# Kernel optimization log

Hardware: AMD Instinct MI355X
Metric: run time of the kernel (lower is better)

## Reference

```python
import jax, jax.numpy as jnp
import numpy as np

N_NODES = 50000
N_EDGES = 800000
NEG_SLOPE = 0.2  # PyG GATv2Conv default
EPS = 1e-16      # PyG softmax denominator epsilon


def _segment_softmax(logits, seg, num_segments):
    # logits: [E, H]; seg: [E] target-node ids
    m = jax.ops.segment_max(logits, seg, num_segments=num_segments)
    p = jnp.exp(logits - m[seg])
    s = jax.ops.segment_sum(p, seg, num_segments=num_segments)
    return p / (s[seg] + EPS)


def _gatv2_conv(x, src, dst, Wl, Wr, att, bias, heads, out_ch, concat):
    # x: [N, F]; Wl/Wr: [F, heads*out_ch]; att: [heads, out_ch]
    n = x.shape[0]
    xl = (x @ Wl).reshape(n, heads, out_ch)
    xr = (x @ Wr).reshape(n, heads, out_ch)
    # GATv2: e_ij = att . leaky_relu(xl[j] + xr[i]) for edge j->i
    e = jax.nn.leaky_relu(xl[src] + xr[dst], NEG_SLOPE)  # [E, H, C]
    logit = jnp.einsum('ehc,hc->eh', e, att)             # [E, H]
    alpha = _segment_softmax(logit, dst, n)              # [E, H]
    out = jax.ops.segment_sum(alpha[:, :, None] * xl[src], dst, num_segments=n)  # [N, H, C]
    if concat:
        out = out.reshape(n, heads * out_ch)
    else:
        out = out.mean(axis=1)
    return out + bias


def setup_inputs() -> dict:
    key = jax.random.key(0)
    ks = jax.random.split(key, 20)
    in_ch, hid, out_ch, heads, edge_dim = 128, 128, 64, 8, 6
    c1 = hid // heads  # 16
    g = lambda k, shp, fan: (jax.random.normal(k, shp, jnp.float32) / np.sqrt(fan)).astype(jnp.float32)
    inp = {
        'x': jax.random.normal(ks[0], (N_NODES, in_ch), jnp.float32),
        'edge_index': jax.random.randint(ks[1], (2, N_EDGES), 0, N_NODES, dtype=jnp.int64),
        'edge_attr': jax.random.normal(ks[2], (N_EDGES, edge_dim), jnp.float32),
        'Wl1': g(ks[3], (in_ch, heads * c1), in_ch),
        'Wr1': g(ks[4], (in_ch, heads * c1), in_ch),
        'att1': g(ks[5], (heads, c1), c1),
        'b1': jnp.zeros((heads * c1,), jnp.float32),
        # layer 2: GATv2Conv(hid -> out_ch, heads=1, no concat)
        'Wl2': g(ks[6], (hid, out_ch), hid),
        'Wr2': g(ks[7], (hid, out_ch), hid),
        'att2': g(ks[8], (1, out_ch), out_ch),
        'b2': jnp.zeros((out_ch,), jnp.float32),
        # edge encoder (computed but unused downstream, as in the source)
        'We1': g(ks[9], (edge_dim, hid), edge_dim), 'be1': jnp.zeros((hid,), jnp.float32),
        'We2': g(ks[10], (hid, hid), hid), 'be2': jnp.zeros((hid,), jnp.float32),
        # classifier
        'Wc1': g(ks[11], (out_ch, hid), out_ch), 'bc1': jnp.zeros((hid,), jnp.float32),
        'Wc2': g(ks[12], (hid, 2), hid), 'bc2': jnp.zeros((2,), jnp.float32),
    }
    return inp


def reference(x, edge_index, edge_attr, Wl1, Wr1, att1, b1, Wl2, Wr2, att2, b2,
              We1, be1, We2, be2, Wc1, bc1, Wc2, bc2):
    n = x.shape[0]
    # edge encoder (dead code in the original forward; kept for fidelity)
    _edge_feats = jax.nn.relu(edge_attr @ We1 + be1) @ We2 + be2
    # add self-loops (PyG GATv2Conv default add_self_loops=True)
    loop = jnp.arange(n, dtype=edge_index.dtype)
    src = jnp.concatenate([edge_index[0], loop])
    dst = jnp.concatenate([edge_index[1], loop])
    # layer 1 (heads=8, concat) + relu; dropout is identity in eval
    h = _gatv2_conv(x, src, dst, Wl1, Wr1, att1, b1, heads=8, out_ch=16, concat=True)
    h = jax.nn.relu(h)
    # layer 2 (heads=1, mean)
    emb = _gatv2_conv(h, src, dst, Wl2, Wr2, att2, b2, heads=1, out_ch=64, concat=False)
    logits = jax.nn.relu(emb @ Wc1 + bc1) @ Wc2 + bc2
    return emb, logits
```

## Files before the change

kernel.cpp:

```cpp
#include <hip/hip_runtime.h>
#include <hip/hip_bf16.h>
#include <cfloat>

#define N_NODES 50000
#define N_EDGES 800000
#define E_TOT   850000
#define NEG_SLOPE 0.2f
#define SM_EPS 1e-16f
#define SCAN_B 196
#define LOG2E 1.4426950408889634f

#define NCH 32
#define CSZ 25000
#define NR  8
#define RSZ 6250

typedef __attribute__((ext_vector_type(8))) short short8;
typedef __attribute__((ext_vector_type(4))) float f32x4;

__device__ __forceinline__ float lrelu(float v) { return v > 0.0f ? v : NEG_SLOPE * v; }

__device__ __forceinline__ unsigned f2bf_pack2(float a, float b) {
    unsigned ua = __float_as_uint(a);
    ua += 0x7fff + ((ua >> 16) & 1);
    unsigned ub = __float_as_uint(b);
    ub += 0x7fff + ((ub >> 16) & 1);
    return (ua >> 16) | (ub & 0xffff0000u);
}
__device__ __forceinline__ unsigned short f2bf(float a) {
    unsigned ua = __float_as_uint(a);
    ua += 0x7fff + ((ua >> 16) & 1);
    return (unsigned short)(ua >> 16);
}
__device__ __forceinline__ float bf_lo(unsigned u) { return __uint_as_float(u << 16); }
__device__ __forceinline__ float bf_hi(unsigned u) { return __uint_as_float(u & 0xffff0000u); }

__device__ __forceinline__ unsigned short pack_one(const float* __restrict__ B0,
                                                   const float* __restrict__ B1,
                                                   int i, int N) {
    int m   = i / (128 * N);
    int rem = i % (128 * N);
    int j    = rem & 7;
    int quad = (rem >> 3) & 3;
    int n    = (rem >> 5) & 15;
    int ctk  = rem >> 9;
    int ct   = ctk % (N / 16);
    int kt   = ctk / (N / 16);
    int k    = kt * 32 + quad * 8 + j;
    int col  = ct * 16 + n;
    const float* B = m ? B1 : B0;
    return f2bf(B[k * N + col]);
}

__global__ void prep(const float* __restrict__ Wl1, const float* __restrict__ Wr1,
                     const float* __restrict__ Wl2, const float* __restrict__ Wr2,
                     const float* __restrict__ Wc1,
                     unsigned short* __restrict__ Bp1, unsigned short* __restrict__ Bp2,
                     unsigned short* __restrict__ Wc1p,
                     int* __restrict__ flags) {
    int i = blockIdx.x * 256 + threadIdx.x;
    if (i < 32768) {
        Bp1[i] = pack_one(Wl1, Wr1, i, 128);
    } else if (i < 49152) {
        Bp2[i - 32768] = pack_one(Wl2, Wr2, i - 32768, 64);
    } else if (i < 57344) {
        int idx = i - 49152;
        int j    = idx & 7;
        int quad = (idx >> 3) & 3;
        int n    = (idx >> 5) & 15;
        int ctk  = idx >> 9;
        int ct   = ctk & 7;
        int kt   = ctk >> 3;
        Wc1p[idx] = f2bf(Wc1[(kt * 32 + quad * 8 + j) * 128 + ct * 16 + n]);
    } else if (i < 57600) {
        flags[i - 57344] = 0;
    }
}

__device__ __forceinline__ void gemm128_both(int b, const float* __restrict__ x,
                                             const unsigned short* __restrict__ Bp1,
                                             unsigned short* __restrict__ xlbf,
                                             float* __restrict__ xr1, int M) {
    int w = threadIdx.x >> 6, lane = threadIdx.x & 63;
    int quad = lane >> 4, l16 = lane & 15;
    int row0 = b * 32 + (w & 1) * 16;
    int cb   = (w >> 1) * 64;
    f32x4 accL[4], accR[4];
    #pragma unroll
    for (int t = 0; t < 4; ++t) {
        accL[t] = (f32x4){0.f, 0.f, 0.f, 0.f};
        accR[t] = (f32x4){0.f, 0.f, 0.f, 0.f};
    }
    int arow = row0 + l16;
    bool aok = arow < M;
    #pragma unroll
    for (int kt = 0; kt < 4; ++kt) {
        short8 a = (short8)0;
        if (aok) {
            const float* Ap = x + (size_t)arow * 128 + quad * 8 + kt * 32;
            float4 f0 = *(const float4*)(Ap);
            float4 f1 = *(const float4*)(Ap + 4);
            union { uint4 u; short8 s; } cv;
            cv.u.x = f2bf_pack2(f0.x, f0.y);
            cv.u.y = f2bf_pack2(f0.z, f0.w);
            cv.u.z = f2bf_pack2(f1.x, f1.y);
            cv.u.w = f2bf_pack2(f1.z, f1.w);
            a = cv.s;
        }
        #pragma unroll
        for (int t = 0; t < 4; ++t) {
            int ct = (cb >> 4) + t;
            const short* bp = (const short*)Bp1 + (((kt * 8 + ct) * 16 + l16) * 4 + quad) * 8;
            short8 bL = *(const short8*)bp;
            short8 bR = *(const short8*)(bp + 128 * 128);
            accL[t] = __builtin_amdgcn_mfma_f32_16x16x32_bf16(a, bL, accL[t], 0, 0, 0);
            accR[t] = __builtin_amdgcn_mfma_f32_16x16x32_bf16(a, bR, accR[t], 0, 0, 0);
        }
    }
    #pragma unroll
    for (int t = 0; t < 4; ++t) {
        int col = cb + t * 16 + l16;
        #pragma unroll
        for (int r = 0; r < 4; ++r) {
            int row = row0 + quad * 4 + r;
            if (row < M) {
                xlbf[(size_t)row * 128 + col] = f2bf(accL[t][r]);
                xr1[(size_t)row * 128 + col]  = accR[t][r];
            }
        }
    }
}

__global__ __launch_bounds__(256)
void k2_count_gemms(const int* __restrict__ ei, unsigned* __restrict__ hist,
                    unsigned short* __restrict__ rank16,
                    const float* __restrict__ x, const unsigned short* __restrict__ Bp1,
                    unsigned short* __restrict__ xlbf, float* __restrict__ xr1, int M) {
    __shared__ unsigned hcnt[RSZ];
    int b = blockIdx.x;
    if (b < NR * NCH) {
        int r = b >> 5, c = b & 31;
        for (int i = threadIdx.x; i < RSZ; i += 256) hcnt[i] = 0;
        int nz = __syncthreads_or(ei[2 * threadIdx.x + 1]);
        int nlo = r * RSZ, nhi = nlo + RSZ;
        int cbeg = c * CSZ, cend = cbeg + CSZ;
        for (int e = cbeg + (int)threadIdx.x; e < cend; e += 1024) {
            int dd[4];
            #pragma unroll
            for (int j = 0; j < 4; ++j) {
                int ee = e + j * 256;
                dd[j] = -1;
                if (ee < cend)
                    dd[j] = nz ? ei[N_EDGES + ee] : ei[2 * N_EDGES + 2 * ee];
            }
            #pragma unroll
            for (int j = 0; j < 4; ++j) {
                int d = dd[j];
                if (d >= nlo && d < nhi) {
                    unsigned rk = atomicAdd(&hcnt[d - nlo], 1u);
                    rank16[e + j * 256] = (unsigned short)rk;
                }
            }
        }
        __syncthreads();
        unsigned* hp = hist + (size_t)(r * NCH + c) * RSZ;
        for (int i = threadIdx.x; i < RSZ; i += 256) hp[i] = hcnt[i];
    } else {
        gemm128_both(b - NR * NCH, x, Bp1, xlbf, xr1, M);
    }
}

__global__ void scan_fused(const unsigned* __restrict__ hist, int* __restrict__ rowptr,
                           int* __restrict__ esrc, int* __restrict__ bsum,
                           int* __restrict__ flags, int* __restrict__ base) {
    __shared__ int sh[256];
    int b = blockIdx.x, t = threadIdx.x, i = b * 256 + t;
    unsigned d[NCH];
    int tot = 0;
    int rr = 0, q = 0;
    if (i < N_NODES) {
        rr = i / RSZ; q = i - rr * RSZ;
        const unsigned* hp = hist + (size_t)rr * NCH * RSZ + q;
        #pragma unroll
        for (int c = 0; c < NCH; ++c) { d[c] = hp[(size_t)c * RSZ]; tot += (int)d[c]; }
    }
    int v = (i < N_NODES) ? tot + 1 : 0;
    sh[t] = v;
    __syncthreads();
    int val = v;
    for (int off = 1; off < 256; off <<= 1) {
        int add = (t >= off) ? sh[t - off] : 0;
        __syncthreads();
        val += add; sh[t] = val;
        __syncthreads();
    }
    if (t == 255) {
        bsum[b] = val;
        __threadfence();
        atomicExch(&flags[b], 1);
    }
    int contrib = 0;
    if (t < b) {
        while (atomicAdd(&flags[t], 0) == 0) {}
        contrib = atomicAdd(&bsum[t], 0);
    }
    __syncthreads();
    sh[t] = contrib;
    __syncthreads();
    #pragma unroll
    for (int off = 128; off; off >>= 1) {
        if (t < off) sh[t] += sh[t + off];
        __syncthreads();
    }
    int offset = sh[0];
    if (i < N_NODES) {
        int rp = (val - v) + offset;
        rowptr[i] = rp;
        esrc[rp] = i;
        int acc = rp + 1;
        int* bp = base + (size_t)rr * NCH * RSZ + q;
        #pragma unroll
        for (int c = 0; c < NCH; ++c) { bp[(size_t)c * RSZ] = acc; acc += (int)d[c]; }
    }
    if (i == 0) rowptr[N_NODES] = E_TOT;
}

__global__ void scatter_edges(const int* __restrict__ ei, const int* __restrict__ base,
                              const unsigned short* __restrict__ rank16,
                              int* __restrict__ esrc) {
    int nz = __syncthreads_or(ei[2 * threadIdx.x + 1]);
    int i = blockIdx.x * blockDim.x + threadIdx.x;
    if (2 * i >= N_EDGES) return;
    bool has2 = (2 * i + 1 < N_EDGES);
    int s0, d0, s1 = 0, d1 = 0;
    if (nz) {
        int2 sp = *(const int2*)(ei + 2 * i);
        int2 dp = *(const int2*)(ei + N_EDGES + 2 * i);
        s0 = sp.x; s1 = sp.y; d0 = dp.x; d1 = dp.y;
    } else {
        int4 sp = *(const int4*)(ei + 4 * i);
        int4 dp = *(const int4*)(ei + 2 * N_EDGES + 4 * i);
        s0 = sp.x; s1 = sp.z; d0 = dp.x; d1 = dp.z;
    }
    unsigned rr = *(const unsigned*)(rank16 + 2 * i);
    int e0 = 2 * i, e1 = 2 * i + 1;
    int c0 = e0 / CSZ, c1 = e1 / CSZ;
    int r0 = d0 / RSZ, r1 = d1 / RSZ;
    esrc[base[((size_t)r0 * NCH + c0) * RSZ + (d0 - r0 * RSZ)] + (int)(rr & 0xffffu)] = s0;
    if (has2)
        esrc[base[((size_t)r1 * NCH + c1) * RSZ + (d1 - r1 * RSZ)] + (int)(rr >> 16)] = s1;
}

__global__ __launch_bounds__(256)
void gemm_mfma64(const unsigned short* __restrict__ Abf, const unsigned short* __restrict__ Bp,
                 unsigned short* __restrict__ C0bf, float* __restrict__ C1, int M) {
    int w = threadIdx.x >> 6, lane = threadIdx.x & 63;
    int quad = lane >> 4, l16 = lane & 15;
    int matrix = w >> 1;
    int row0 = blockIdx.x * 32 + (w & 1) * 16;
    const unsigned short* Bm = Bp + matrix * 128 * 64;
    f32x4 acc[4];
    #pragma unroll
    for (int t = 0; t < 4; ++t) acc[t] = (f32x4){0.f, 0.f, 0.f, 0.f};
    int arow = row0 + l16;
    bool aok = arow < M;
    const short* Ap = (const short*)Abf + (size_t)arow * 128 + quad * 8;
    #pragma unroll
    for (int kt = 0; kt < 4; ++kt) {
        short8 a = (short8)0;
        if (aok) a = *(const short8*)(Ap + kt * 32);
        #pragma unroll
        for (int t = 0; t < 4; ++t) {
            const short* bp = (const short*)Bm + (((kt * 4 + t) * 16 + l16) * 4 + quad) * 8;
            short8 bfr = *(const short8*)bp;
            acc[t] = __builtin_amdgcn_mfma_f32_16x16x32_bf16(a, bfr, acc[t], 0, 0, 0);
        }
    }
    #pragma unroll
    for (int t = 0; t < 4; ++t) {
        int col = t * 16 + l16;
        #pragma unroll
        for (int r = 0; r < 4; ++r) {
            int row = row0 + quad * 4 + r;
            if (row < M) {
                if (matrix) C1[(size_t)row * 64 + col] = acc[t][r];
                else        C0bf[(size_t)row * 64 + col] = f2bf(acc[t][r]);
            }
        }
    }
}

__global__ __launch_bounds__(256)
void node_fused1(const int* __restrict__ rowptr, const int* __restrict__ esrc,
                 const unsigned short* __restrict__ xlbf, const float* __restrict__ xr,
                 const float* __restrict__ att, const float* __restrict__ b1,
                 unsigned short* __restrict__ hbf) {
    int wave = threadIdx.x >> 6;
    int lane = threadIdx.x & 63;
    int n = blockIdx.x * 4 + wave;
    int slot = lane >> 4;
    int l = lane & 15;
    int beg = rowptr[n], end = rowptr[n + 1];
    const float* xrp = xr + (size_t)n * 128 + 8 * l;
    float4 xra = *(const float4*)(xrp);
    float4 xrb = *(const float4*)(xrp + 4);
    float4 ata = *(const float4*)(att + 8 * l);
    float4 atb = *(const float4*)(att + 8 * l + 4);
    ata.x *= LOG2E; ata.y *= LOG2E; ata.z *= LOG2E; ata.w *= LOG2E;
    atb.x *= LOG2E; atb.y *= LOG2E; atb.z *= LOG2E; atb.w *= LOG2E;
    float den = 0.0f;
    float4 aa = {0, 0, 0, 0}, ab = {0, 0, 0, 0};

    auto body = [&](int k) {
        int s = esrc[k];
        uint4 u = *(const uint4*)(xlbf + (size_t)s * 128 + 8 * l);
        float x0 = bf_lo(u.x), x1 = bf_hi(u.x);
        float x2 = bf_lo(u.y), x3 = bf_hi(u.y);
        float x4 = bf_lo(u.z), x5 = bf_hi(u.z);
        float x6 = bf_lo(u.w), x7 = bf_hi(u.w);
        float v = ata.x * lrelu(x0 + xra.x) + ata.y * lrelu(x1 + xra.y)
                + ata.z * lrelu(x2 + xra.z) + ata.w * lrelu(x3 + xra.w)
                + atb.x * lrelu(x4 + xrb.x) + atb.y * lrelu(x5 + xrb.y)
                + atb.z * lrelu(x6 + xrb.z) + atb.w * lrelu(x7 + xrb.w);
        v += __shfl_xor(v, 1);
        float p = exp2f(v);
        den += p;
        aa.x += p * x0; aa.y += p * x1; aa.z += p * x2; aa.w += p * x3;
        ab.x += p * x4; ab.y += p * x5; ab.z += p * x6; ab.w += p * x7;
    };
    int k = beg + slot;
    for (; k + 4 < end; k += 8) { body(k); body(k + 4); }
    if (k < end) body(k);

    #pragma unroll
    for (int off = 16; off < 64; off <<= 1) {
        aa.x += __shfl_xor(aa.x, off); aa.y += __shfl_xor(aa.y, off);
        aa.z += __shfl_xor(aa.z, off); aa.w += __shfl_xor(aa.w, off);
        ab.x += __shfl_xor(ab.x, off); ab.y += __shfl_xor(ab.y, off);
        ab.z += __shfl_xor(ab.z, off); ab.w += __shfl_xor(ab.w, off);
        den   += __shfl_xor(den, off);
    }
    if (slot == 0) {
        float inv = 1.0f / (den + SM_EPS);
        float4 b4a = *(const float4*)(b1 + 8 * l);
        float4 b4b = *(const float4*)(b1 + 8 * l + 4);
        float oa0 = fmaxf(aa.x * inv + b4a.x, 0.0f);
        float oa1 = fmaxf(aa.y * inv + b4a.y, 0.0f);
        float oa2 = fmaxf(aa.z * inv + b4a.z, 0.0f);
        float oa3 = fmaxf(aa.w * inv + b4a.w, 0.0f);
        float ob0 = fmaxf(ab.x * inv + b4b.x, 0.0f);
        float ob1 = fmaxf(ab.y * inv + b4b.y, 0.0f);
        float ob2 = fmaxf(ab.z * inv + b4b.z, 0.0f);
        float ob3 = fmaxf(ab.w * inv + b4b.w, 0.0f);
        uint4 pk;
        pk.x = f2bf_pack2(oa0, oa1);
        pk.y = f2bf_pack2(oa2, oa3);
        pk.z = f2bf_pack2(ob0, ob1);
        pk.w = f2bf_pack2(ob2, ob3);
        *(uint4*)(hbf + (size_t)n * 128 + 8 * l) = pk;
    }
}

__global__ __launch_bounds__(256)
void node_fused2(const int* __restrict__ rowptr, const int* __restrict__ esrc,
                 const unsigned short* __restrict__ xlbf, const float* __restrict__ xr,
                 const float* __restrict__ att, const float* __restrict__ b2v,
                 float* __restrict__ out_emb, unsigned short* __restrict__ embbf) {
    int wave = threadIdx.x >> 6;
    int lane = threadIdx.x & 63;
    int n = blockIdx.x * 4 + wave;
    int slot = lane >> 3;
    int l = lane & 7;
    int beg = rowptr[n], end = rowptr[n + 1];
    const float* xrp = xr + (size_t)n * 64 + 8 * l;
    float4 xra = *(const float4*)(xrp);
    float4 xrb = *(const float4*)(xrp + 4);
    float4 ata = *(const float4*)(att + 8 * l);
    float4 atb = *(const float4*)(att + 8 * l + 4);
    ata.x *= LOG2E; ata.y *= LOG2E; ata.z *= LOG2E; ata.w *= LOG2E;
    atb.x *= LOG2E; atb.y *= LOG2E; atb.z *= LOG2E; atb.w *= LOG2E;
    float den = 0.0f;
    float4 aa = {0, 0, 0, 0}, ab = {0, 0, 0, 0};

    auto body = [&](int k) {
        int s = esrc[k];
        uint4 u = *(const uint4*)(xlbf + (size_t)s * 64 + 8 * l);
        float x0 = bf_lo(u.x), x1 = bf_hi(u.x);
        float x2 = bf_lo(u.y), x3 = bf_hi(u.y);
        float x4 = bf_lo(u.z), x5 = bf_hi(u.z);
        float x6 = bf_lo(u.w), x7 = bf_hi(u.w);
        float v = ata.x * lrelu(x0 + xra.x) + ata.y * lrelu(x1 + xra.y)
                + ata.z * lrelu(x2 + xra.z) + ata.w * lrelu(x3 + xra.w)
                + atb.x * lrelu(x4 + xrb.x) + atb.y * lrelu(x5 + xrb.y)
                + atb.z * lrelu(x6 + xrb.z) + atb.w * lrelu(x7 + xrb.w);
        v += __shfl_xor(v, 1);
        v += __shfl_xor(v, 2);
        v += __shfl_xor(v, 4);
        float p = exp2f(v);
        den += p;
        aa.x += p * x0; aa.y += p * x1; aa.z += p * x2; aa.w += p * x3;
        ab.x += p * x4; ab.y += p * x5; ab.z += p * x6; ab.w += p * x7;
    };
    int k = beg + slot;
    for (; k + 8 < end; k += 16) { body(k); body(k + 8); }
    if (k < end) body(k);

    #pragma unroll
    for (int off = 8; off < 64; off <<= 1) {
        aa.x += __shfl_xor(aa.x, off); aa.y += __shfl_xor(aa.y, off);
        aa.z += __shfl_xor(aa.z, off); aa.w += __shfl_xor(aa.w, off);
        ab.x += __shfl_xor(ab.x, off); ab.y += __shfl_xor(ab.y, off);
        ab.z += __shfl_xor(ab.z, off); ab.w += __shfl_xor(ab.w, off);
        den   += __shfl_xor(den, off);
    }
    if (slot == 0) {
        float inv = 1.0f / (den + SM_EPS);
        float4 b4a = *(const float4*)(b2v + 8 * l);
        float4 b4b = *(const float4*)(b2v + 8 * l + 4);
        float4 ea, eb;
        ea.x = aa.x * inv + b4a.x; ea.y = aa.y * inv + b4a.y;
        ea.z = aa.z * inv + b4a.z; ea.w = aa.w * inv + b4a.w;
        eb.x = ab.x * inv + b4b.x; eb.y = ab.y * inv + b4b.y;
        eb.z = ab.z * inv + b4b.z; eb.w = ab.w * inv + b4b.w;
        float* op = out_emb + (size_t)n * 64 + 8 * l;
        *(float4*)(op)     = ea;
        *(float4*)(op + 4) = eb;
        uint4 pk;
        pk.x = f2bf_pack2(ea.x, ea.y);
        pk.y = f2bf_pack2(ea.z, ea.w);
        pk.z = f2bf_pack2(eb.x, eb.y);
        pk.w = f2bf_pack2(eb.z, eb.w);
        *(uint4*)(embbf + (size_t)n * 64 + 8 * l) = pk;
    }
}

__global__ __launch_bounds__(256)
void cls_mfma(const unsigned short* __restrict__ embbf, const unsigned short* __restrict__ Wc1p,
              const float* __restrict__ bc1, const float* __restrict__ Wc2,
              const float* __restrict__ bc2, float* __restrict__ out_logits) {
    __shared__ float part[2][16][2][2];
    int w = threadIdx.x >> 6, lane = threadIdx.x & 63;
    int quad = lane >> 4, l16 = lane & 15;
    int rowhalf = w & 1, colhalf = w >> 1;
    int row0 = blockIdx.x * 32 + rowhalf * 16;
    int cb = colhalf * 64;
    f32x4 acc[4];
    #pragma unroll
    for (int t = 0; t < 4; ++t) acc[t] = (f32x4){0.f, 0.f, 0.f, 0.f};
    int arow = row0 + l16;
    bool aok = arow < N_NODES;
    const short* Ap = (const short*)embbf + (size_t)arow * 64 + quad * 8;
    #pragma unroll
    for (int kt = 0; kt < 2; ++kt) {
        short8 a = (short8)0;
        if (aok) a = *(const short8*)(Ap + kt * 32);
        #pragma unroll
        for (int t = 0; t < 4; ++t) {
            int ct = colhalf * 4 + t;
            const short* bp = (const short*)Wc1p + (((kt * 8 + ct) * 16 + l16) * 4 + quad) * 8;
            short8 bfr = *(const short8*)bp;
            acc[t] = __builtin_amdgcn_mfma_f32_16x16x32_bf16(a, bfr, acc[t], 0, 0, 0);
        }
    }
    float p0[4] = {0, 0, 0, 0}, p1[4] = {0, 0, 0, 0};
    #pragma unroll
    for (int t = 0; t < 4; ++t) {
        int col = cb + t * 16 + l16;
        float w2a = Wc2[2 * col], w2b = Wc2[2 * col + 1];
        float bc = bc1[col];
        #pragma unroll
        for (int r = 0; r < 4; ++r) {
            float tv = fmaxf(acc[t][r] + bc, 0.0f);
            p0[r] += tv * w2a;
            p1[r] += tv * w2b;
        }
    }
    #pragma unroll
    for (int off = 1; off < 16; off <<= 1) {
        #pragma unroll
        for (int r = 0; r < 4; ++r) {
            p0[r] += __shfl_xor(p0[r], off);
            p1[r] += __shfl_xor(p1[r], off);
        }
    }
    if (l16 == 0) {
        #pragma unroll
        for (int r = 0; r < 4; ++r) {
            part[rowhalf][quad * 4 + r][colhalf][0] = p0[r];
            part[rowhalf][quad * 4 + r][colhalf][1] = p1[r];
        }
    }
    __syncthreads();
    int t = threadIdx.x;
    if (t < 64) {
        int row = t >> 1, c = t & 1;
        int rh = row >> 4, r16 = row & 15;
        float s = part[rh][r16][0][c] + part[rh][r16][1][c] + bc2[c];
        int n = blockIdx.x * 32 + row;
        if (n < N_NODES) out_logits[(size_t)n * 2 + c] = s;
    }
}

extern "C" void kernel_launch(void* const* d_in, const int* in_sizes, int n_in,
                              void* d_out, int out_size, void* d_ws, size_t ws_size,
                              hipStream_t stream) {
    const float* x    = (const float*)d_in[0];
    const int*   ei   = (const int*)d_in[1];
    const float* Wl1  = (const float*)d_in[3];
    const float* Wr1  = (const float*)d_in[4];
    const float* att1 = (const float*)d_in[5];
    const float* b1   = (const float*)d_in[6];
    const float* Wl2  = (const float*)d_in[7];
    const float* Wr2  = (const float*)d_in[8];
    const float* att2 = (const float*)d_in[9];
    const float* b2   = (const float*)d_in[10];
    const float* Wc1  = (const float*)d_in[15];
    const float* bc1  = (const float*)d_in[16];
    const float* Wc2  = (const float*)d_in[17];
    const float* bc2  = (const float*)d_in[18];

    float* ws = (float*)d_ws;
    int* rowptr = (int*)ws + 50000;
    int* esrc   = rowptr + 50016;
    int* bsum   = esrc + 850000;
    int* flags  = bsum + 256;
    unsigned short* rank16 = (unsigned short*)(flags + 256);
    float* xr1           = ws + 1400448;
    unsigned short* xlbf = (unsigned short*)(ws + 7800448);
    unsigned short* hbf  = (unsigned short*)(ws + 11000448);
    unsigned* hist = (unsigned*)(ws + 11000448);
    int* base      = (int*)(ws + 12600448);
    unsigned short* Bp1   = (unsigned short*)(ws + 14200448);
    unsigned short* Bp2   = (unsigned short*)(ws + 14216832);
    unsigned short* Wc1p  = (unsigned short*)(ws + 14225024);
    unsigned short* embbf = (unsigned short*)(ws + 14229120);

    float* out_emb    = (float*)d_out;
    float* out_logits = out_emb + (size_t)N_NODES * 64;

    prep<<<225, 256, 0, stream>>>(Wl1, Wr1, Wl2, Wr2, Wc1, Bp1, Bp2, Wc1p, flags);

    k2_count_gemms<<<256 + 1563, 256, 0, stream>>>(ei, hist, rank16, x, Bp1, xlbf, xr1, N_NODES);

    scan_fused<<<SCAN_B, 256, 0, stream>>>(hist, rowptr, esrc, bsum, flags, base);

    scatter_edges<<<1563, 256, 0, stream>>>(ei, base, rank16, esrc);

    node_fused1<<<12500, 256, 0, stream>>>(rowptr, esrc, xlbf, xr1, att1, b1, hbf);

    gemm_mfma64<<<1563, 256, 0, stream>>>(hbf, Bp2, xlbf, xr1, N_NODES);
    node_fused2<<<12500, 256, 0, stream>>>(rowptr, esrc, xlbf, xr1, att2, b2, out_emb, embbf);

    cls_mfma<<<1563, 256, 0, stream>>>(embbf, Wc1p, bc1, Wc2, bc2, out_logits);
}
```

Baseline: 287.0 us.

## Widen per-lane channel tiles, prefetch gathers, use packed FMA leaky-relu in GAT aggregation

Both node aggregation kernels now give each lane 16 channels instead of 8, which doubles the edges processed in parallel per wave and cuts shuffle reductions. Layer 1 no longer needs the cross-lane logit shuffle, and layer 2 needs one fewer. The edge loop software-prefetches the next source row and the index after it, to hide gather latency. Leaky-relu is rewritten as 0.6*t + 0.4*|t| with packed f32x2 FMAs, so the math can use packed VALU ops. The cost is more registers per lane and a larger final cross-slot reduction.

```diff
diff --git a/kernel.cpp b/kernel.cpp
--- a/kernel.cpp
+++ b/kernel.cpp
@@ -17,6 +17,7 @@
 
 typedef __attribute__((ext_vector_type(8))) short short8;
 typedef __attribute__((ext_vector_type(4))) float f32x4;
+typedef __attribute__((ext_vector_type(2))) float f32x2;
 
 __device__ __forceinline__ float lrelu(float v) { return v > 0.0f ? v : NEG_SLOPE * v; }
 
@@ -34,6 +35,18 @@
 }
 __device__ __forceinline__ float bf_lo(unsigned u) { return __uint_as_float(u << 16); }
 __device__ __forceinline__ float bf_hi(unsigned u) { return __uint_as_float(u & 0xffff0000u); }
+__device__ __forceinline__ f32x2 bf_unpk(unsigned u) {
+    f32x2 r;
+    r.x = __uint_as_float(u << 16);
+    r.y = __uint_as_float(u & 0xffff0000u);
+    return r;
+}
+__device__ __forceinline__ f32x2 fabs2(f32x2 a) {
+    f32x2 r;
+    r.x = __uint_as_float(__float_as_uint(a.x) & 0x7fffffffu);
+    r.y = __uint_as_float(__float_as_uint(a.y) & 0x7fffffffu);
+    return r;
+}
 
 __device__ __forceinline__ unsigned short pack_one(const float* __restrict__ B0,
                                                    const float* __restrict__ B1,
@@ -298,66 +311,81 @@
     int wave = threadIdx.x >> 6;
     int lane = threadIdx.x & 63;
     int n = blockIdx.x * 4 + wave;
-    int slot = lane >> 4;
-    int l = lane & 15;
+    int slot = lane >> 3;
+    int h = lane & 7;
     int beg = rowptr[n], end = rowptr[n + 1];
-    const float* xrp = xr + (size_t)n * 128 + 8 * l;
-    float4 xra = *(const float4*)(xrp);
-    float4 xrb = *(const float4*)(xrp + 4);
-    float4 ata = *(const float4*)(att + 8 * l);
-    float4 atb = *(const float4*)(att + 8 * l + 4);
-    ata.x *= LOG2E; ata.y *= LOG2E; ata.z *= LOG2E; ata.w *= LOG2E;
-    atb.x *= LOG2E; atb.y *= LOG2E; atb.z *= LOG2E; atb.w *= LOG2E;
+    const float* xrp = xr + (size_t)n * 128 + 16 * h;
+    f32x2 xrv[8];
+    #pragma unroll
+    for (int j = 0; j < 8; ++j) xrv[j] = *(const f32x2*)(xrp + 2 * j);
+    const float* atp = att + 16 * h;
+    const float c6 = 0.6f * LOG2E, c4 = 0.4f * LOG2E;
+    f32x2 a6[8], a4[8];
+    #pragma unroll
+    for (int j = 0; j < 8; ++j) {
+        f32x2 a = *(const f32x2*)(atp + 2 * j);
+        a6[j] = a * c6;
+        a4[j] = a * c4;
+    }
     float den = 0.0f;
-    float4 aa = {0, 0, 0, 0}, ab = {0, 0, 0, 0};
-
-    auto body = [&](int k) {
-        int s = esrc[k];
-        uint4 u = *(const uint4*)(xlbf + (size_t)s * 128 + 8 * l);
-        float x0 = bf_lo(u.x), x1 = bf_hi(u.x);
-        float x2 = bf_lo(u.y), x3 = bf_hi(u.y);
-        float x4 = bf_lo(u.z), x5 = bf_hi(u.z);
-        float x6 = bf_lo(u.w), x7 = bf_hi(u.w);
-        float v = ata.x * lrelu(x0 + xra.x) + ata.y * lrelu(x1 + xra.y)
-                + ata.z * lrelu(x2 + xra.z) + ata.w * lrelu(x3 + xra.w)
-                + atb.x * lrelu(x4 + xrb.x) + atb.y * lrelu(x5 + xrb.y)
-                + atb.z * lrelu(x6 + xrb.z) + atb.w * lrelu(x7 + xrb.w);
-        v += __shfl_xor(v, 1);
-        float p = exp2f(v);
+    f32x2 acc[8];
+    #pragma unroll
+    for (int j = 0; j < 8; ++j) acc[j] = (f32x2){0.f, 0.f};
+
+    auto ld0 = [&](int s) -> uint4 { return *(const uint4*)(xlbf + (size_t)s * 128 + 16 * h); };
+    auto ld1 = [&](int s) -> uint4 { return *(const uint4*)(xlbf + (size_t)s * 128 + 16 * h + 8); };
+    int k0 = beg + slot;
+    int sA = esrc[k0 < end ? k0 : beg];
+    int sB = esrc[k0 + 8 < end ? k0 + 8 : beg];
+    uint4 uA0 = ld0(sA), uA1 = ld1(sA);
+
+    for (int k = k0; k < end; k += 8) {
+        uint4 uN0 = ld0(sB), uN1 = ld1(sB);
+        int sN = esrc[k + 16 < end ? k + 16 : beg];
+        unsigned uu[8] = {uA0.x, uA0.y, uA0.z, uA0.w, uA1.x, uA1.y, uA1.z, uA1.w};
+        f32x2 xv[8];
+        f32x2 v2 = {0.f, 0.f};
+        #pragma unroll
+        for (int j = 0; j < 8; ++j) {
+            xv[j] = bf_unpk(uu[j]);
+            f32x2 t = xv[j] + xrv[j];
+            v2 = __builtin_elementwise_fma(a6[j], t, v2);
+            v2 = __builtin_elementwise_fma(a4[j], fabs2(t), v2);
+        }
+        float p = exp2f(v2.x + v2.y);
         den += p;
-        aa.x += p * x0; aa.y += p * x1; aa.z += p * x2; aa.w += p * x3;
-        ab.x += p * x4; ab.y += p * x5; ab.z += p * x6; ab.w += p * x7;
-    };
-    int k = beg + slot;
-    for (; k + 4 < end; k += 8) { body(k); body(k + 4); }
-    if (k < end) body(k);
-
-    #pragma unroll
-    for (int off = 16; off < 64; off <<= 1) {
-        aa.x += __shfl_xor(aa.x, off); aa.y += __shfl_xor(aa.y, off);
-        aa.z += __shfl_xor(aa.z, off); aa.w += __shfl_xor(aa.w, off);
-        ab.x += __shfl_xor(ab.x, off); ab.y += __shfl_xor(ab.y, off);
-        ab.z += __shfl_xor(ab.z, off); ab.w += __shfl_xor(ab.w, off);
-        den   += __shfl_xor(den, off);
+        f32x2 p2 = {p, p};
+        #pragma unroll
+        for (int j = 0; j < 8; ++j) acc[j] = __builtin_elementwise_fma(p2, xv[j], acc[j]);
+        uA0 = uN0; uA1 = uN1; sB = sN;
+    }
+
+    #pragma unroll
+    for (int off = 8; off < 64; off <<= 1) {
+        #pragma unroll
+        for (int j = 0; j < 8; ++j) {
+            acc[j].x += __shfl_xor(acc[j].x, off);
+            acc[j].y += __shfl_xor(acc[j].y, off);
+        }
+        den += __shfl_xor(den, off);
     }
     if (slot == 0) {
         float inv = 1.0f / (den + SM_EPS);
-        float4 b4a = *(const float4*)(b1 + 8 * l);
-        float4 b4b = *(const float4*)(b1 + 8 * l + 4);
-        float oa0 = fmaxf(aa.x * inv + b4a.x, 0.0f);
-        float oa1 = fmaxf(aa.y * inv + b4a.y, 0.0f);
-        float oa2 = fmaxf(aa.z * inv + b4a.z, 0.0f);
-        float oa3 = fmaxf(aa.w * inv + b4a.w, 0.0f);
-        float ob0 = fmaxf(ab.x * inv + b4b.x, 0.0f);
-        float ob1 = fmaxf(ab.y * inv + b4b.y, 0.0f);
-        float ob2 = fmaxf(ab.z * inv + b4b.z, 0.0f);
-        float ob3 = fmaxf(ab.w * inv + b4b.w, 0.0f);
-        uint4 pk;
-        pk.x = f2bf_pack2(oa0, oa1);
-        pk.y = f2bf_pack2(oa2, oa3);
-        pk.z = f2bf_pack2(ob0, ob1);
-        pk.w = f2bf_pack2(ob2, ob3);
-        *(uint4*)(hbf + (size_t)n * 128 + 8 * l) = pk;
+        const float* bp = b1 + 16 * h;
+        float o[16];
+        #pragma unroll
+        for (int j = 0; j < 8; ++j) {
+            o[2 * j]     = fmaxf(__builtin_fmaf(acc[j].x, inv, bp[2 * j]), 0.0f);
+            o[2 * j + 1] = fmaxf(__builtin_fmaf(acc[j].y, inv, bp[2 * j + 1]), 0.0f);
+        }
+        uint4 pk0, pk1;
+        pk0.x = f2bf_pack2(o[0], o[1]);   pk0.y = f2bf_pack2(o[2], o[3]);
+        pk0.z = f2bf_pack2(o[4], o[5]);   pk0.w = f2bf_pack2(o[6], o[7]);
+        pk1.x = f2bf_pack2(o[8], o[9]);   pk1.y = f2bf_pack2(o[10], o[11]);
+        pk1.z = f2bf_pack2(o[12], o[13]); pk1.w = f2bf_pack2(o[14], o[15]);
+        unsigned short* hp = hbf + (size_t)n * 128 + 16 * h;
+        *(uint4*)(hp)     = pk0;
+        *(uint4*)(hp + 8) = pk1;
     }
 }
 
@@ -369,68 +397,90 @@
     int wave = threadIdx.x >> 6;
     int lane = threadIdx.x & 63;
     int n = blockIdx.x * 4 + wave;
-    int slot = lane >> 3;
-    int l = lane & 7;
+    int slot = lane >> 2;
+    int cl = lane & 3;
     int beg = rowptr[n], end = rowptr[n + 1];
-    const float* xrp = xr + (size_t)n * 64 + 8 * l;
-    float4 xra = *(const float4*)(xrp);
-    float4 xrb = *(const float4*)(xrp + 4);
-    float4 ata = *(const float4*)(att + 8 * l);
-    float4 atb = *(const float4*)(att + 8 * l + 4);
-    ata.x *= LOG2E; ata.y *= LOG2E; ata.z *= LOG2E; ata.w *= LOG2E;
-    atb.x *= LOG2E; atb.y *= LOG2E; atb.z *= LOG2E; atb.w *= LOG2E;
+    const float* xrp = xr + (size_t)n * 64 + 16 * cl;
+    f32x2 xrv[8];
+    #pragma unroll
+    for (int j = 0; j < 8; ++j) xrv[j] = *(const f32x2*)(xrp + 2 * j);
+    const float* atp = att + 16 * cl;
+    const float c6 = 0.6f * LOG2E, c4 = 0.4f * LOG2E;
+    f32x2 a6[8], a4[8];
+    #pragma unroll
+    for (int j = 0; j < 8; ++j) {
+        f32x2 a = *(const f32x2*)(atp + 2 * j);
+        a6[j] = a * c6;
+        a4[j] = a * c4;
+    }
     float den = 0.0f;
-    float4 aa = {0, 0, 0, 0}, ab = {0, 0, 0, 0};
-
-    auto body = [&](int k) {
-        int s = esrc[k];
-        uint4 u = *(const uint4*)(xlbf + (size_t)s * 64 + 8 * l);
-        float x0 = bf_lo(u.x), x1 = bf_hi(u.x);
-        float x2 = bf_lo(u.y), x3 = bf_hi(u.y);
-        float x4 = bf_lo(u.z), x5 = bf_hi(u.z);
-        float x6 = bf_lo(u.w), x7 = bf_hi(u.w);
-        float v = ata.x * lrelu(x0 + xra.x) + ata.y * lrelu(x1 + xra.y)
-                + ata.z * lrelu(x2 + xra.z) + ata.w * lrelu(x3 + xra.w)
-                + atb.x * lrelu(x4 + xrb.x) + atb.y * lrelu(x5 + xrb.y)
-                + atb.z * lrelu(x6 + xrb.z) + atb.w * lrelu(x7 + xrb.w);
+    f32x2 acc[8];
+    #pragma unroll
+    for (int j = 0; j < 8; ++j) acc[j] = (f32x2){0.f, 0.f};
+
+    auto ld0 = [&](int s) -> uint4 { return *(const uint4*)(xlbf + (size_t)s * 64 + 16 * cl); };
+    auto ld1 = [&](int s) -> uint4 { return *(const uint4*)(xlbf + (size_t)s * 64 + 16 * cl + 8); };
+    int k0 = beg + slot;
+    int sA = esrc[k0 < end ? k0 : beg];
+    int sB = esrc[k0 + 16 < end ? k0 + 16 : beg];
+    uint4 uA0 = ld0(sA), uA1 = ld1(sA);
+
+    for (int k = k0; k < end; k += 16) {
+        uint4 uN0 = ld0(sB), uN1 = ld1(sB);
+        int sN = esrc[k + 32 < end ? k + 32 : beg];
+        unsigned uu[8] = {uA0.x, uA0.y, uA0.z, uA0.w, uA1.x, uA1.y, uA1.z, uA1.w};
+        f32x2 xv[8];
+        f32x2 v2 = {0.f, 0.f};
+        #pragma unroll
+        for (int j = 0; j < 8; ++j) {
+            xv[j] = bf_unpk(uu[j]);
+            f32x2 t = xv[j] + xrv[j];
+            v2 = __builtin_elementwise_fma(a6[j], t, v2);
+            v2 = __builtin_elementwise_fma(a4[j], fabs2(t), v2);
+        }
+        float v = v2.x + v2.y;
         v += __shfl_xor(v, 1);
         v += __shfl_xor(v, 2);
-        v += __shfl_xor(v, 4);
         float p = exp2f(v);
         den += p;
-        aa.x += p * x0; aa.y += p * x1; aa.z += p * x2; aa.w += p * x3;
-        ab.x += p * x4; ab.y += p * x5; ab.z += p * x6; ab.w += p * x7;
-    };
-    int k = beg + slot;
-    for (; k + 8 < end; k += 16) { body(k); body(k + 8); }
-    if (k < end) body(k);
-
-    #pragma unroll
-    for (int off = 8; off < 64; off <<= 1) {
-        aa.x += __shfl_xor(aa.x, off); aa.y += __shfl_xor(aa.y, off);
-        aa.z += __shfl_xor(aa.z, off); aa.w += __shfl_xor(aa.w, off);
-        ab.x += __shfl_xor(ab.x, off); ab.y += __shfl_xor(ab.y, off);
-        ab.z += __shfl_xor(ab.z, off); ab.w += __shfl_xor(ab.w, off);
-        den   += __shfl_xor(den, off);
+        f32x2 p2 = {p, p};
+        #pragma unroll
+        for (int j = 0; j < 8; ++j) acc[j] = __builtin_elementwise_fma(p2, xv[j], acc[j]);
+        uA0 = uN0; uA1 = uN1; sB = sN;
+    }
+
+    #pragma unroll
+    for (int off = 4; off < 64; off <<= 1) {
+        #pragma unroll
+        for (int j = 0; j < 8; ++j) {
+            acc[j].x += __shfl_xor(acc[j].x, off);
+            acc[j].y += __shfl_xor(acc[j].y, off);
+        }
+        den += __shfl_xor(den, off);
     }
     if (slot == 0) {
         float inv = 1.0f / (den + SM_EPS);
-        float4 b4a = *(const float4*)(b2v + 8 * l);
-        float4 b4b = *(const float4*)(b2v + 8 * l + 4);
-        float4 ea, eb;
-        ea.x = aa.x * inv + b4a.x; ea.y = aa.y * inv + b4a.y;
-        ea.z = aa.z * inv + b4a.z; ea.w = aa.w * inv + b4a.w;
-        eb.x = ab.x * inv + b4b.x; eb.y = ab.y * inv + b4b.y;
-        eb.z = ab.z * inv + b4b.z; eb.w = ab.w * inv + b4b.w;
-        float* op = out_emb + (size_t)n * 64 + 8 * l;
-        *(float4*)(op)     = ea;
-        *(float4*)(op + 4) = eb;
-        uint4 pk;
-        pk.x = f2bf_pack2(ea.x, ea.y);
-        pk.y = f2bf_pack2(ea.z, ea.w);
-        pk.z = f2bf_pack2(eb.x, eb.y);
-        pk.w = f2bf_pack2(eb.z, eb.w);
-        *(uint4*)(embbf + (size_t)n * 64 + 8 * l) = pk;
+        const float* bp = b2v + 16 * cl;
+        float o[16];
+        #pragma unroll
+        for (int j = 0; j < 8; ++j) {
+            o[2 * j]     = __builtin_fmaf(acc[j].x, inv, bp[2 * j]);
+            o[2 * j + 1] = __builtin_fmaf(acc[j].y, inv, bp[2 * j + 1]);
+        }
+        float* op = out_emb + (size_t)n * 64 + 16 * cl;
+        #pragma unroll
+        for (int j = 0; j < 4; ++j) {
+            float4 f; f.x = o[4 * j]; f.y = o[4 * j + 1]; f.z = o[4 * j + 2]; f.w = o[4 * j + 3];
+            *(float4*)(op + 4 * j) = f;
+        }
+        uint4 pk0, pk1;
+        pk0.x = f2bf_pack2(o[0], o[1]);   pk0.y = f2bf_pack2(o[2], o[3]);
+        pk0.z = f2bf_pack2(o[4], o[5]);   pk0.w = f2bf_pack2(o[6], o[7]);
+        pk1.x = f2bf_pack2(o[8], o[9]);   pk1.y = f2bf_pack2(o[10], o[11]);
+        pk1.z = f2bf_pack2(o[12], o[13]); pk1.w = f2bf_pack2(o[14], o[15]);
+        unsigned short* ep = embbf + (size_t)n * 64 + 16 * cl;
+        *(uint4*)(ep)     = pk0;
+        *(uint4*)(ep + 8) = pk1;
     }
 }
 
```

New measurement: 327.6 us. 14.1% more time.
